# Performance work log

Hardware: AMD Instinct MI355X
Metric: run time of the kernel (lower is better)

The kernel has to match this reference:

```python
import jax, jax.numpy as jnp
import numpy as np

N_NODES = 100000
N_EDGES = 800000
IN_DIM = 64
HID = 96
OUT_DIM = 1
N_LAYERS = 3
N_CENTRAL = 512
BN_EPS = 1e-5


def setup_inputs() -> dict:
    key = jax.random.key(0)
    ks = jax.random.split(key, 16)
    s = 0.1  # weight scale to keep activations tame
    return {
        "x": jax.random.normal(ks[0], (N_NODES, IN_DIM), jnp.float32),
        "edge_index": jax.random.randint(ks[1], (2, N_EDGES), 0, N_NODES, jnp.int64 if jax.config.jax_enable_x64 else jnp.int32),
        "batch": jnp.zeros((N_NODES,), jnp.int32),
        "central_node_idx": jax.random.randint(ks[2], (N_CENTRAL,), 0, N_NODES, jnp.int32),
        "W_emb": jax.random.normal(ks[3], (IN_DIM, HID), jnp.float32) * s,
        "b_emb": jax.random.normal(ks[4], (HID,), jnp.float32) * s,
        "conv_wl": jax.random.normal(ks[5], (N_LAYERS, HID, HID), jnp.float32) * s,
        "conv_bl": jax.random.normal(ks[6], (N_LAYERS, HID), jnp.float32) * s,
        "conv_wr": jax.random.normal(ks[7], (N_LAYERS, HID, HID), jnp.float32) * s,
        "bn_gamma": jnp.ones((N_LAYERS, HID), jnp.float32),
        "bn_beta": jnp.zeros((N_LAYERS, HID), jnp.float32),
        "W1": jax.random.normal(ks[8], (HID, HID), jnp.float32) * s,
        "b1": jax.random.normal(ks[9], (HID,), jnp.float32) * s,
        "W2": jax.random.normal(ks[10], (HID, OUT_DIM), jnp.float32) * s,
        "b2": jax.random.normal(ks[11], (OUT_DIM,), jnp.float32) * s,
    }


def _sage_mean_agg(h, src, dst, n):
    # PyG SAGEConv mean aggregation: mean of source features at each target node
    msg = h[src]                                             # [E, H] gather
    summed = jax.ops.segment_sum(msg, dst, num_segments=n)   # [N, H] scatter-add
    deg = jax.ops.segment_sum(jnp.ones((src.shape[0],), h.dtype), dst, num_segments=n)
    return summed / jnp.maximum(deg, 1.0)[:, None]


def reference(x, edge_index, batch, central_node_idx, W_emb, b_emb,
              conv_wl, conv_bl, conv_wr, bn_gamma, bn_beta, W1, b1, W2, b2):
    n = x.shape[0]
    src, dst = edge_index[0], edge_index[1]
    h = jax.nn.relu(x @ W_emb + b_emb)                       # [N, H]
    for i in range(conv_wl.shape[0]):
        agg = _sage_mean_agg(h, src, dst, n)
        # SAGEConv: lin_l(agg) (with bias) + lin_r(x_root) (no bias)
        h = agg @ conv_wl[i] + conv_bl[i] + h @ conv_wr[i]
        # BatchNorm1d, training mode: batch stats with biased variance
        mean = h.mean(axis=0)
        var = h.var(axis=0)
        h = (h - mean) * jax.lax.rsqrt(var + BN_EPS) * bn_gamma[i] + bn_beta[i]
        h = jax.nn.relu(h)
    central = h[central_node_idx]                            # [G, H]
    out = jax.nn.relu(central @ W1 + b1) @ W2 + b2           # [G, OUT]
    return out
```

## Files before the change

kernel.cpp:

```cpp
#include <hip/hip_runtime.h>

#define NN 100000
#define NE 800000
#define IND 64
#define HID 96
#define NL 3
#define NC 512
#define BN_EPS 1e-5f

#define NBE ((NN + 127) / 128)
#define NBP (NL * 9)
#define NBH ((NE + 4095) / 4096)
#define NBF ((NE + 4095) / 4096)
#define NBK2 196
#define BCAP 4864

typedef __attribute__((ext_vector_type(8))) short bf16x8;
typedef __attribute__((ext_vector_type(4))) float f32x4;

static __device__ __forceinline__ float b2f(ushort u) {
    union { uint i; float f; } v; v.i = ((uint)u) << 16; return v.f;
}
static __device__ __forceinline__ ushort f2b(float f) {
    union { float f; uint i; } v; v.f = f;
    uint r = v.i + 0x7FFFu + ((v.i >> 16) & 1u);
    return (ushort)(r >> 16);
}
static __device__ __forceinline__ uint pack2(float a, float b) {
    return (uint)f2b(a) | ((uint)f2b(b) << 16);
}

static __device__ __forceinline__ void prep_one(const float* srcA, const float* srcB,
                                                ushort* dst, int t) {
    int lane = t & 63;
    int ct = (t >> 6) % 6;
    int kt = t / (6 * 64);
    int k0 = kt * 32 + (lane >> 4) * 8;
    int col = ct * 16 + (lane & 15);
    ushort tmp[8];
#pragma unroll
    for (int j = 0; j < 8; ++j) {
        int k = k0 + j;
        const float* src = (srcB == nullptr || k < 96) ? srcA : srcB;
        int kk = (srcB == nullptr || k < 96) ? k : k - 96;
        tmp[j] = f2b(src[kk * HID + col]);
    }
    uint* od = (uint*)(dst + (size_t)t * 8);
    od[0] = (uint)tmp[0] | ((uint)tmp[1] << 16);
    od[1] = (uint)tmp[2] | ((uint)tmp[3] << 16);
    od[2] = (uint)tmp[4] | ((uint)tmp[5] << 16);
    od[3] = (uint)tmp[6] | ((uint)tmp[7] << 16);
}

__global__ __launch_bounds__(256) void k_front(const float* __restrict__ x,
        const float* __restrict__ W_emb, const float* __restrict__ bias,
        ushort* __restrict__ h,
        const float* __restrict__ conv_wl, const float* __restrict__ conv_wr,
        ushort* __restrict__ Bfl,
        const int* __restrict__ ei, int* __restrict__ hist,
        int* __restrict__ gcur, uint* __restrict__ part) {
    __shared__ __align__(16) char smem[24576];
    const int b = blockIdx.x;
    const int tid = threadIdx.x;
    if (b >= NBE) {
        if (b < NBE + NBP) {
            int idx = b - NBE;
            int l = idx / 9, bb = idx % 9;
            int t = bb * 256 + tid;
            if (t < 6 * 6 * 64)
                prep_one(conv_wl + (size_t)l * 9216, conv_wr + (size_t)l * 9216,
                         Bfl + (size_t)l * 18432, t);
        } else if (b < NBE + NBP + NBH) {
            int base = (b - NBE - NBP) * 4096;
            for (int i = tid; i < 4096; i += 256) {
                int e = base + i;
                if (e < NE) atomicAdd(&hist[ei[NE + e]], 1);
            }
        } else {
            uint* ordbuf = (uint*)smem;
            unsigned char* sbk = (unsigned char*)(smem + 16384);
            int* lhist = (int*)(smem + 20480);
            int* lscan = (int*)(smem + 21504);
            int* lbase = (int*)(smem + 22528);
            int* lcnt2 = (int*)(smem + 23552);
            const int base_e = (b - NBE - NBP - NBH) * 4096;
            lhist[tid] = 0; lcnt2[tid] = 0;
            __syncthreads();
#pragma unroll
            for (int it = 0; it < 16; ++it) {
                int e = base_e + it * 256 + tid;
                if (e < NE) atomicAdd(&lhist[ei[NE + e] >> 9], 1);
            }
            __syncthreads();
            int v = lhist[tid];
            lscan[tid] = v;
            __syncthreads();
            for (int off = 1; off < 256; off <<= 1) {
                int t2 = (tid >= off) ? lscan[tid - off] : 0;
                __syncthreads();
                lscan[tid] += t2;
                __syncthreads();
            }
            int excl = lscan[tid] - v;
            __syncthreads();
            lscan[tid] = excl;
            if (v > 0) lbase[tid] = atomicAdd(&gcur[tid], v);
            __syncthreads();
#pragma unroll
            for (int it = 0; it < 16; ++it) {
                int e = base_e + it * 256 + tid;
                if (e < NE) {
                    int s = ei[e], d = ei[NE + e];
                    int bk = d >> 9;
                    int lofs = atomicAdd(&lcnt2[bk], 1);
                    int slot = lscan[bk] + lofs;
                    ordbuf[slot] = (uint)s | ((uint)(d & 511) << 17);
                    sbk[slot] = (unsigned char)bk;
                }
            }
            __syncthreads();
            int total = NE - base_e; if (total > 4096) total = 4096;
            for (int i = tid; i < total; i += 256) {
                int bk = sbk[i];
                part[(size_t)bk * BCAP + lbase[bk] + (i - lscan[bk])] = ordbuf[i];
            }
        }
        return;
    }
    ushort* sB = (ushort*)smem;
    ushort* sT = (ushort*)smem;
    for (int i = tid; i < 768; i += 256) {
        int lane = i & 63;
        int ct = (i >> 6) % 6;
        int kt = i / (6 * 64);
        int k0 = kt * 32 + (lane >> 4) * 8;
        int col = ct * 16 + (lane & 15);
        ushort tmp[8];
#pragma unroll
        for (int j = 0; j < 8; ++j) tmp[j] = f2b(W_emb[(k0 + j) * HID + col]);
        uint4 o;
        o.x = (uint)tmp[0] | ((uint)tmp[1] << 16);
        o.y = (uint)tmp[2] | ((uint)tmp[3] << 16);
        o.z = (uint)tmp[4] | ((uint)tmp[5] << 16);
        o.w = (uint)tmp[6] | ((uint)tmp[7] << 16);
        ((uint4*)sB)[i] = o;
    }
    __syncthreads();
    const int wave = tid >> 6, lane = tid & 63;
    const int rowb = wave * 32;
    const int row0 = b * 128 + rowb;
    const int kof = (lane >> 4) * 8;
    f32x4 acc[2][6];
#pragma unroll
    for (int t = 0; t < 2; ++t)
#pragma unroll
        for (int c = 0; c < 6; ++c) acc[t][c] = (f32x4){0.f, 0.f, 0.f, 0.f};
#pragma unroll
    for (int kt = 0; kt < 2; ++kt) {
        int kk = kt * 32 + kof;
        bf16x8 a[2];
#pragma unroll
        for (int t = 0; t < 2; ++t) {
            int r = row0 + t * 16 + (lane & 15);
            if (r >= NN) r = NN - 1;
            const float* src = x + (size_t)r * IND + kk;
            float4 f0 = *(const float4*)src;
            float4 f1 = *(const float4*)(src + 4);
            a[t][0] = (short)f2b(f0.x); a[t][1] = (short)f2b(f0.y);
            a[t][2] = (short)f2b(f0.z); a[t][3] = (short)f2b(f0.w);
            a[t][4] = (short)f2b(f1.x); a[t][5] = (short)f2b(f1.y);
            a[t][6] = (short)f2b(f1.z); a[t][7] = (short)f2b(f1.w);
        }
#pragma unroll
        for (int ct = 0; ct < 6; ++ct) {
            bf16x8 bb = *(const bf16x8*)&sB[((kt * 6 + ct) * 64 + lane) * 8];
            acc[0][ct] = __builtin_amdgcn_mfma_f32_16x16x32_bf16(a[0], bb, acc[0][ct], 0, 0, 0);
            acc[1][ct] = __builtin_amdgcn_mfma_f32_16x16x32_bf16(a[1], bb, acc[1][ct], 0, 0, 0);
        }
    }
    __syncthreads();
#pragma unroll
    for (int t = 0; t < 2; ++t)
#pragma unroll
        for (int ct = 0; ct < 6; ++ct) {
            int col = ct * 16 + (lane & 15);
            float bv = bias[col];
#pragma unroll
            for (int i = 0; i < 4; ++i) {
                int rb = rowb + t * 16 + (lane >> 4) * 4 + i;
                float v = acc[t][ct][i] + bv;
                sT[rb * HID + col] = f2b(v > 0.f ? v : 0.f);
            }
        }
    __syncthreads();
    for (int i = tid; i < 1536; i += 256) {
        int r = i / 12;
        int g = b * 128 + r;
        if (g < NN) ((uint4*)(h + (size_t)g * HID))[i % 12] = ((uint4*)sT)[i];
    }
}

__global__ __launch_bounds__(1024) void k_scan1(const int* __restrict__ hist,
        int* __restrict__ rp, int* __restrict__ bsum) {
    __shared__ int sd[1024];
    const int tid = threadIdx.x;
    const int i = blockIdx.x * 1024 + tid;
    int v = (i < NN) ? hist[i] : 0;
    sd[tid] = v;
    __syncthreads();
    for (int off = 1; off < 1024; off <<= 1) {
        int t = (tid >= off) ? sd[tid - off] : 0;
        __syncthreads();
        sd[tid] += t;
        __syncthreads();
    }
    if (i < NN) rp[i] = sd[tid] - v;
    if (tid == 1023) bsum[blockIdx.x] = sd[1023];
}

__global__ __launch_bounds__(128) void k_scan2(const int* __restrict__ bsum,
                                               int* __restrict__ boff) {
    __shared__ int sd[128];
    const int tid = threadIdx.x;
    const int NB = (NN + 1023) / 1024;
    int v = (tid < NB) ? bsum[tid] : 0;
    sd[tid] = v;
    __syncthreads();
    for (int off = 1; off < 128; off <<= 1) {
        int t = (tid >= off) ? sd[tid - off] : 0;
        __syncthreads();
        sd[tid] += t;
        __syncthreads();
    }
    if (tid < NB) boff[tid] = sd[tid] - v;
}

__global__ __launch_bounds__(1024) void k_scan3(int* __restrict__ rp,
        const int* __restrict__ boff) {
    const int i = blockIdx.x * 1024 + threadIdx.x;
    if (i < NN) rp[i] += boff[blockIdx.x];
    if (i == 0) rp[NN] = NE;
}

__global__ __launch_bounds__(256) void k_fill2(const uint* __restrict__ part,
        const int* __restrict__ gcur, const int* __restrict__ rp,
        int* __restrict__ col) {
    __shared__ int lcur[512];
    const int tid = threadIdx.x;
    const int bk = blockIdx.x;
    const int n0 = bk * 512;
    for (int i = tid; i < 512; i += 256) {
        int n = n0 + i;
        lcur[i] = (n < NN) ? rp[n] : 0;
    }
    __syncthreads();
    const int cnt = gcur[bk];
    const uint* pb = part + (size_t)bk * BCAP;
    for (int e = tid; e < cnt; e += 256) {
        uint v = pb[e];
        int pos = atomicAdd(&lcur[v >> 17], 1);
        col[pos] = (int)(v & 0x1FFFF);
    }
}

__global__ __launch_bounds__(256) void k_agg(const ushort* __restrict__ pre,
        const int* __restrict__ rp, const int* __restrict__ col,
        const float* __restrict__ stats, const float* __restrict__ gamma,
        const float* __restrict__ beta, ushort* __restrict__ agg) {
    __shared__ float sc[96], sh[96];
    const int tid = threadIdx.x;
    if (tid < 96) {
        float scv = 1.f, shv = 0.f;
        if (stats) {
            float mean = stats[tid] * (1.f / NN);
            float var  = stats[96 + tid] * (1.f / NN) - mean * mean;
            float s = gamma[tid] * rsqrtf(var + BN_EPS);
            scv = s; shv = beta[tid] - mean * s;
        }
        sc[tid] = scv; sh[tid] = shv;
    }
    __syncthreads();
    const int lane = tid & 15;
    const int n = blockIdx.x * 16 + (tid >> 4);
    if (n >= NN) return;
    const float s0a = sc[2*lane],      h0a = sh[2*lane];
    const float s0b = sc[2*lane + 1],  h0b = sh[2*lane + 1];
    const float s1a = sc[2*lane + 32], h1a = sh[2*lane + 32];
    const float s1b = sc[2*lane + 33], h1b = sh[2*lane + 33];
    const float s2a = sc[2*lane + 64], h2a = sh[2*lane + 64];
    const float s2b = sc[2*lane + 65], h2b = sh[2*lane + 65];
    const int e0 = rp[n], e1 = rp[n + 1];
    float a0 = 0.f, a1 = 0.f, a2 = 0.f, a3 = 0.f, a4 = 0.f, a5 = 0.f;
    const uint* hu = (const uint*)pre;
    int e = e0;
    for (; e + 8 <= e1; e += 8) {
        uint u[8][3];
#pragma unroll
        for (int i = 0; i < 8; ++i) {
            const uint* r = hu + (size_t)col[e + i] * 48 + lane;
            u[i][0] = r[0]; u[i][1] = r[16]; u[i][2] = r[32];
        }
#pragma unroll
        for (int i = 0; i < 8; ++i) {
            a0 += fmaxf(b2f((ushort)u[i][0])         * s0a + h0a, 0.f);
            a1 += fmaxf(b2f((ushort)(u[i][0] >> 16)) * s0b + h0b, 0.f);
            a2 += fmaxf(b2f((ushort)u[i][1])         * s1a + h1a, 0.f);
            a3 += fmaxf(b2f((ushort)(u[i][1] >> 16)) * s1b + h1b, 0.f);
            a4 += fmaxf(b2f((ushort)u[i][2])         * s2a + h2a, 0.f);
            a5 += fmaxf(b2f((ushort)(u[i][2] >> 16)) * s2b + h2b, 0.f);
        }
    }
    for (; e + 4 <= e1; e += 4) {
        uint u[4][3];
#pragma unroll
        for (int i = 0; i < 4; ++i) {
            const uint* r = hu + (size_t)col[e + i] * 48 + lane;
            u[i][0] = r[0]; u[i][1] = r[16]; u[i][2] = r[32];
        }
#pragma unroll
        for (int i = 0; i < 4; ++i) {
            a0 += fmaxf(b2f((ushort)u[i][0])         * s0a + h0a, 0.f);
            a1 += fmaxf(b2f((ushort)(u[i][0] >> 16)) * s0b + h0b, 0.f);
            a2 += fmaxf(b2f((ushort)u[i][1])         * s1a + h1a, 0.f);
            a3 += fmaxf(b2f((ushort)(u[i][1] >> 16)) * s1b + h1b, 0.f);
            a4 += fmaxf(b2f((ushort)u[i][2])         * s2a + h2a, 0.f);
            a5 += fmaxf(b2f((ushort)(u[i][2] >> 16)) * s2b + h2b, 0.f);
        }
    }
    for (; e < e1; ++e) {
        const uint* r = hu + (size_t)col[e] * 48 + lane;
        uint u0 = r[0], u1 = r[16], u2 = r[32];
        a0 += fmaxf(b2f((ushort)u0)         * s0a + h0a, 0.f);
        a1 += fmaxf(b2f((ushort)(u0 >> 16)) * s0b + h0b, 0.f);
        a2 += fmaxf(b2f((ushort)u1)         * s1a + h1a, 0.f);
        a3 += fmaxf(b2f((ushort)(u1 >> 16)) * s1b + h1b, 0.f);
        a4 += fmaxf(b2f((ushort)u2)         * s2a + h2a, 0.f);
        a5 += fmaxf(b2f((ushort)(u2 >> 16)) * s2b + h2b, 0.f);
    }
    int d = e1 - e0; if (d < 1) d = 1;
    float inv = 1.0f / (float)d;
    uint* ar = (uint*)agg + (size_t)n * 48 + lane;
    ar[0]  = pack2(a0 * inv, a1 * inv);
    ar[16] = pack2(a2 * inv, a3 * inv);
    ar[32] = pack2(a4 * inv, a5 * inv);
}

__global__ __launch_bounds__(256, 4) void k_gemm(const ushort* __restrict__ aggb,
        const ushort* __restrict__ pre, const ushort* __restrict__ Bf,
        const float* __restrict__ bl, ushort* __restrict__ hnew,
        float* __restrict__ stats,
        const float* __restrict__ statsP, const float* __restrict__ gammaP,
        const float* __restrict__ betaP) {
    __shared__ __align__(16) char smem[40704];
    ushort* sB = (ushort*)smem;
    ushort* sT = (ushort*)smem;
    float*  sredS = (float*)(smem + 36864);
    float*  sredQ = (float*)(smem + 38400);
    float2* sscsh = (float2*)(smem + 39936);
    const int tid = threadIdx.x;
    for (int i = tid; i < 2304; i += 256) ((uint4*)sB)[i] = ((const uint4*)Bf)[i];
    if (tid < 96) {
        float scv = 1.f, shv = 0.f;
        if (statsP) {
            float mean = statsP[tid] * (1.f / NN);
            float var  = statsP[96 + tid] * (1.f / NN) - mean * mean;
            float s = gammaP[tid] * rsqrtf(var + BN_EPS);
            scv = s; shv = betaP[tid] - mean * s;
        }
        sscsh[tid] = make_float2(scv, shv);
    }
    __syncthreads();
    const int wave = tid >> 6, lane = tid & 63;
    const int rowb = wave * 32;
    const int row0 = blockIdx.x * 128 + rowb;
    const int kof = (lane >> 4) * 8;
    f32x4 acc[2][6];
#pragma unroll
    for (int t = 0; t < 2; ++t)
#pragma unroll
        for (int c = 0; c < 6; ++c) acc[t][c] = (f32x4){0.f, 0.f, 0.f, 0.f};
#pragma unroll
    for (int kt = 0; kt < 6; ++kt) {
        bf16x8 a[2];
#pragma unroll
        for (int t = 0; t < 2; ++t) {
            int r = row0 + t * 16 + (lane & 15);
            if (r >= NN) r = NN - 1;
            if (kt < 3) {
                int kk = kt * 32 + kof;
                a[t] = *(const bf16x8*)(aggb + (size_t)r * HID + kk);
            } else {
                int kk = (kt - 3) * 32 + kof;
                bf16x8 raw = *(const bf16x8*)(pre + (size_t)r * HID + kk);
                union { bf16x8 h; uint u[4]; } pk;
#pragma unroll
                for (int j = 0; j < 4; ++j) {
                    float2 p0 = sscsh[kk + 2*j];
                    float2 p1 = sscsh[kk + 2*j + 1];
                    float v0 = fmaxf(b2f((ushort)raw[2*j])     * p0.x + p0.y, 0.f);
                    float v1 = fmaxf(b2f((ushort)raw[2*j + 1]) * p1.x + p1.y, 0.f);
                    pk.u[j] = pack2(v0, v1);
                }
                a[t] = pk.h;
            }
        }
#pragma unroll
        for (int ct = 0; ct < 6; ++ct) {
            bf16x8 bb = *(const bf16x8*)&sB[((kt * 6 + ct) * 64 + lane) * 8];
            acc[0][ct] = __builtin_amdgcn_mfma_f32_16x16x32_bf16(a[0], bb, acc[0][ct], 0, 0, 0);
            acc[1][ct] = __builtin_amdgcn_mfma_f32_16x16x32_bf16(a[1], bb, acc[1][ct], 0, 0, 0);
        }
    }
    __syncthreads();
    float s[6], q[6];
#pragma unroll
    for (int c = 0; c < 6; ++c) { s[c] = 0.f; q[c] = 0.f; }
#pragma unroll
    for (int t = 0; t < 2; ++t)
#pragma unroll
        for (int ct = 0; ct < 6; ++ct) {
            int col = ct * 16 + (lane & 15);
            float bv = bl[col];
#pragma unroll
            for (int i = 0; i < 4; ++i) {
                int rb = rowb + t * 16 + (lane >> 4) * 4 + i;
                int g = blockIdx.x * 128 + rb;
                float v = acc[t][ct][i] + bv;
                if (g < NN) { s[ct] += v; q[ct] += v * v; }
                sT[rb * HID + col] = f2b(v);
            }
        }
#pragma unroll
    for (int c = 0; c < 6; ++c) {
        s[c] += __shfl_xor(s[c], 16); s[c] += __shfl_xor(s[c], 32);
        q[c] += __shfl_xor(q[c], 16); q[c] += __shfl_xor(q[c], 32);
    }
    if (lane < 16) {
#pragma unroll
        for (int c = 0; c < 6; ++c) {
            sredS[wave * 96 + c * 16 + lane] = s[c];
            sredQ[wave * 96 + c * 16 + lane] = q[c];
        }
    }
    __syncthreads();
    if (tid < 96) {
        float S = sredS[tid] + sredS[96 + tid] + sredS[192 + tid] + sredS[288 + tid];
        float Q = sredQ[tid] + sredQ[96 + tid] + sredQ[192 + tid] + sredQ[288 + tid];
        atomicAdd(&stats[tid], S);
        atomicAdd(&stats[96 + tid], Q);
    }
    for (int i = tid; i < 1536; i += 256) {
        int r = i / 12;
        int g = blockIdx.x * 128 + r;
        if (g < NN) ((uint4*)(hnew + (size_t)g * HID))[i % 12] = ((uint4*)sT)[i];
    }
}

__global__ __launch_bounds__(128) void k_mlp(const ushort* __restrict__ pre,
        const int* __restrict__ cidx, const float* __restrict__ stats,
        const float* __restrict__ gamma, const float* __restrict__ beta,
        const float* __restrict__ W1, const float* __restrict__ b1,
        const float* __restrict__ W2, const float* __restrict__ b2,
        float* __restrict__ out) {
    __shared__ float nh[96];
    __shared__ float hid[96];
    __shared__ float red[128];
    const int c = blockIdx.x;
    const int node = cidx[c];
    const int tid = threadIdx.x;
    if (tid < 96) {
        float mean = stats[tid] * (1.f / NN);
        float var  = stats[96 + tid] * (1.f / NN) - mean * mean;
        float s = gamma[tid] * rsqrtf(var + BN_EPS);
        float v = b2f(pre[(size_t)node * 96 + tid]) * s + (beta[tid] - mean * s);
        nh[tid] = fmaxf(v, 0.f);
    }
    __syncthreads();
    if (tid < 96) {
        float a = 0.f;
        for (int k = 0; k < 96; ++k) a += nh[k] * W1[k * 96 + tid];
        hid[tid] = fmaxf(a + b1[tid], 0.f);
    }
    __syncthreads();
    red[tid] = (tid < 96) ? hid[tid] * W2[tid] : 0.f;
    __syncthreads();
    for (int off = 64; off > 0; off >>= 1) {
        if (tid < off) red[tid] += red[tid + off];
        __syncthreads();
    }
    if (tid == 0) out[c] = red[0] + b2[0];
}

extern "C" void kernel_launch(void* const* d_in, const int* in_sizes, int n_in,
                              void* d_out, int out_size, void* d_ws, size_t ws_size,
                              hipStream_t stream) {
    const float* x        = (const float*)d_in[0];
    const int*   ei       = (const int*)d_in[1];
    const int*   cidx     = (const int*)d_in[3];
    const float* W_emb    = (const float*)d_in[4];
    const float* b_emb    = (const float*)d_in[5];
    const float* conv_wl  = (const float*)d_in[6];
    const float* conv_bl  = (const float*)d_in[7];
    const float* conv_wr  = (const float*)d_in[8];
    const float* bn_gamma = (const float*)d_in[9];
    const float* bn_beta  = (const float*)d_in[10];
    const float* W1       = (const float*)d_in[11];
    const float* b1       = (const float*)d_in[12];
    const float* W2       = (const float*)d_in[13];
    const float* b2       = (const float*)d_in[14];
    float* out = (float*)d_out;

    char* ws = (char*)d_ws;
    size_t off = 0;
    auto alloc = [&](size_t bytes) -> void* {
        void* p = ws + off;
        off = (off + bytes + 255) & ~(size_t)255;
        return p;
    };
    ushort* h    = (ushort*)alloc((size_t)NN * 96 * 2);
    ushort* hnew = (ushort*)alloc((size_t)NN * 96 * 2);
    ushort* agg  = (ushort*)alloc((size_t)NN * 96 * 2);
    int*   hist  = (int*)alloc((size_t)NN * 4);
    int*   gcur  = (int*)alloc(256 * 4);
    int*   rp    = (int*)alloc((size_t)(NN + 1) * 4);
    int*   col   = (int*)alloc((size_t)NE * 4);
    uint*  part  = (uint*)alloc((size_t)NBK2 * BCAP * 4);
    int*   bsum  = (int*)alloc(128 * 4);
    int*   boff  = (int*)alloc(128 * 4);
    float* stats = (float*)alloc((size_t)NL * 192 * 4);
    ushort* Bfl  = (ushort*)alloc((size_t)NL * 6 * 6 * 64 * 8 * 2);
    (void)ws_size; (void)in_sizes; (void)n_in; (void)out_size;

    const int NB = (NN + 1023) / 1024;

    hipMemsetAsync(hist, 0, ((size_t)NN * 4 + 255 & ~(size_t)255) + 256 * 4, stream);
    hipMemsetAsync(stats, 0, (size_t)NL * 192 * 4, stream);

    k_front<<<NBE + NBP + NBH + NBF, 256, 0, stream>>>(x, W_emb, b_emb, h,
        conv_wl, conv_wr, Bfl, ei, hist, gcur, part);
    k_scan1<<<NB, 1024, 0, stream>>>(hist, rp, bsum);
    k_scan2<<<1, 128, 0, stream>>>(bsum, boff);
    k_scan3<<<NB, 1024, 0, stream>>>(rp, boff);
    k_fill2<<<NBK2, 256, 0, stream>>>(part, gcur, rp, col);

    const ushort* src = h;
    ushort* dst = hnew;
    for (int l = 0; l < NL; ++l) {
        const float* stP = (l == 0) ? nullptr : stats + (size_t)(l - 1) * 192;
        const float* gP  = (l == 0) ? nullptr : bn_gamma + (size_t)(l - 1) * 96;
        const float* bP  = (l == 0) ? nullptr : bn_beta + (size_t)(l - 1) * 96;
        k_agg<<<(NN + 15) / 16, 256, 0, stream>>>(src, rp, col, stP, gP, bP, agg);
        k_gemm<<<(NN + 127) / 128, 256, 0, stream>>>(agg, src,
            Bfl + (size_t)l * 18432, conv_bl + (size_t)l * 96, dst,
            stats + (size_t)l * 192, stP, gP, bP);
        const ushort* t = src; src = dst; dst = (ushort*)t;
    }
    k_mlp<<<NC, 128, 0, stream>>>(src, cidx, stats + (size_t)(NL - 1) * 192,
        bn_gamma + (size_t)(NL - 1) * 96, bn_beta + (size_t)(NL - 1) * 96,
        W1, b1, W2, b2, out);
}
```

Before: 271.9 us.

## Fuse mean aggregation into layer GEMM and derive degree histogram from partitions

Merges the per-layer gather/mean aggregation kernel and the MFMA GEMM kernel into one k_layer kernel. Aggregated rows now go into padded shared memory instead of a global bf16 buffer, which removes a full N×96 write and read per layer. The global atomic in-degree histogram pass is replaced by a per-bucket shared-memory histogram built from the already-partitioned edge buckets. B fragments are now read from global memory rather than staged in LDS. The risks are lower gather parallelism per block (128 nodes per 256 threads), possible tail imbalance, and B reads going through cache instead of LDS.

```diff
diff --git a/kernel.cpp b/kernel.cpp
--- a/kernel.cpp
+++ b/kernel.cpp
@@ -10,10 +10,10 @@
 
 #define NBE ((NN + 127) / 128)
 #define NBP (NL * 9)
-#define NBH ((NE + 4095) / 4096)
 #define NBF ((NE + 4095) / 4096)
 #define NBK2 196
 #define BCAP 4864
+#define ATP 52
 
 typedef __attribute__((ext_vector_type(8))) short bf16x8;
 typedef __attribute__((ext_vector_type(4))) float f32x4;
@@ -57,8 +57,8 @@
         ushort* __restrict__ h,
         const float* __restrict__ conv_wl, const float* __restrict__ conv_wr,
         ushort* __restrict__ Bfl,
-        const int* __restrict__ ei, int* __restrict__ hist,
-        int* __restrict__ gcur, uint* __restrict__ part) {
+        const int* __restrict__ ei, int* __restrict__ gcur,
+        uint* __restrict__ part) {
     __shared__ __align__(16) char smem[24576];
     const int b = blockIdx.x;
     const int tid = threadIdx.x;
@@ -70,12 +70,6 @@
             if (t < 6 * 6 * 64)
                 prep_one(conv_wl + (size_t)l * 9216, conv_wr + (size_t)l * 9216,
                          Bfl + (size_t)l * 18432, t);
-        } else if (b < NBE + NBP + NBH) {
-            int base = (b - NBE - NBP) * 4096;
-            for (int i = tid; i < 4096; i += 256) {
-                int e = base + i;
-                if (e < NE) atomicAdd(&hist[ei[NE + e]], 1);
-            }
         } else {
             uint* ordbuf = (uint*)smem;
             unsigned char* sbk = (unsigned char*)(smem + 16384);
@@ -83,7 +77,7 @@
             int* lscan = (int*)(smem + 21504);
             int* lbase = (int*)(smem + 22528);
             int* lcnt2 = (int*)(smem + 23552);
-            const int base_e = (b - NBE - NBP - NBH) * 4096;
+            const int base_e = (b - NBE - NBP) * 4096;
             lhist[tid] = 0; lcnt2[tid] = 0;
             __syncthreads();
 #pragma unroll
@@ -200,6 +194,24 @@
     }
 }
 
+__global__ __launch_bounds__(256) void k_hist2(const uint* __restrict__ part,
+        const int* __restrict__ gcur, int* __restrict__ hist) {
+    __shared__ int lh[512];
+    const int tid = threadIdx.x;
+    const int bk = blockIdx.x;
+    lh[tid] = 0; lh[tid + 256] = 0;
+    __syncthreads();
+    const int cnt = gcur[bk];
+    const uint* pb = part + (size_t)bk * BCAP;
+    for (int e = tid; e < cnt; e += 256) atomicAdd(&lh[pb[e] >> 17], 1);
+    __syncthreads();
+    const int n0 = bk * 512;
+    for (int i = tid; i < 512; i += 256) {
+        int n = n0 + i;
+        if (n < NN) hist[n] = lh[i];
+    }
+}
+
 __global__ __launch_bounds__(1024) void k_scan1(const int* __restrict__ hist,
         int* __restrict__ rp, int* __restrict__ bsum) {
     __shared__ int sd[1024];
@@ -263,102 +275,19 @@
     }
 }
 
-__global__ __launch_bounds__(256) void k_agg(const ushort* __restrict__ pre,
+__global__ __launch_bounds__(256, 4) void k_layer(const ushort* __restrict__ pre,
         const int* __restrict__ rp, const int* __restrict__ col,
-        const float* __restrict__ stats, const float* __restrict__ gamma,
-        const float* __restrict__ beta, ushort* __restrict__ agg) {
-    __shared__ float sc[96], sh[96];
-    const int tid = threadIdx.x;
-    if (tid < 96) {
-        float scv = 1.f, shv = 0.f;
-        if (stats) {
-            float mean = stats[tid] * (1.f / NN);
-            float var  = stats[96 + tid] * (1.f / NN) - mean * mean;
-            float s = gamma[tid] * rsqrtf(var + BN_EPS);
-            scv = s; shv = beta[tid] - mean * s;
-        }
-        sc[tid] = scv; sh[tid] = shv;
-    }
-    __syncthreads();
-    const int lane = tid & 15;
-    const int n = blockIdx.x * 16 + (tid >> 4);
-    if (n >= NN) return;
-    const float s0a = sc[2*lane],      h0a = sh[2*lane];
-    const float s0b = sc[2*lane + 1],  h0b = sh[2*lane + 1];
-    const float s1a = sc[2*lane + 32], h1a = sh[2*lane + 32];
-    const float s1b = sc[2*lane + 33], h1b = sh[2*lane + 33];
-    const float s2a = sc[2*lane + 64], h2a = sh[2*lane + 64];
-    const float s2b = sc[2*lane + 65], h2b = sh[2*lane + 65];
-    const int e0 = rp[n], e1 = rp[n + 1];
-    float a0 = 0.f, a1 = 0.f, a2 = 0.f, a3 = 0.f, a4 = 0.f, a5 = 0.f;
-    const uint* hu = (const uint*)pre;
-    int e = e0;
-    for (; e + 8 <= e1; e += 8) {
-        uint u[8][3];
-#pragma unroll
-        for (int i = 0; i < 8; ++i) {
-            const uint* r = hu + (size_t)col[e + i] * 48 + lane;
-            u[i][0] = r[0]; u[i][1] = r[16]; u[i][2] = r[32];
-        }
-#pragma unroll
-        for (int i = 0; i < 8; ++i) {
-            a0 += fmaxf(b2f((ushort)u[i][0])         * s0a + h0a, 0.f);
-            a1 += fmaxf(b2f((ushort)(u[i][0] >> 16)) * s0b + h0b, 0.f);
-            a2 += fmaxf(b2f((ushort)u[i][1])         * s1a + h1a, 0.f);
-            a3 += fmaxf(b2f((ushort)(u[i][1] >> 16)) * s1b + h1b, 0.f);
-            a4 += fmaxf(b2f((ushort)u[i][2])         * s2a + h2a, 0.f);
-            a5 += fmaxf(b2f((ushort)(u[i][2] >> 16)) * s2b + h2b, 0.f);
-        }
-    }
-    for (; e + 4 <= e1; e += 4) {
-        uint u[4][3];
-#pragma unroll
-        for (int i = 0; i < 4; ++i) {
-            const uint* r = hu + (size_t)col[e + i] * 48 + lane;
-            u[i][0] = r[0]; u[i][1] = r[16]; u[i][2] = r[32];
-        }
-#pragma unroll
-        for (int i = 0; i < 4; ++i) {
-            a0 += fmaxf(b2f((ushort)u[i][0])         * s0a + h0a, 0.f);
-            a1 += fmaxf(b2f((ushort)(u[i][0] >> 16)) * s0b + h0b, 0.f);
-            a2 += fmaxf(b2f((ushort)u[i][1])         * s1a + h1a, 0.f);
-            a3 += fmaxf(b2f((ushort)(u[i][1] >> 16)) * s1b + h1b, 0.f);
-            a4 += fmaxf(b2f((ushort)u[i][2])         * s2a + h2a, 0.f);
-            a5 += fmaxf(b2f((ushort)(u[i][2] >> 16)) * s2b + h2b, 0.f);
-        }
-    }
-    for (; e < e1; ++e) {
-        const uint* r = hu + (size_t)col[e] * 48 + lane;
-        uint u0 = r[0], u1 = r[16], u2 = r[32];
-        a0 += fmaxf(b2f((ushort)u0)         * s0a + h0a, 0.f);
-        a1 += fmaxf(b2f((ushort)(u0 >> 16)) * s0b + h0b, 0.f);
-        a2 += fmaxf(b2f((ushort)u1)         * s1a + h1a, 0.f);
-        a3 += fmaxf(b2f((ushort)(u1 >> 16)) * s1b + h1b, 0.f);
-        a4 += fmaxf(b2f((ushort)u2)         * s2a + h2a, 0.f);
-        a5 += fmaxf(b2f((ushort)(u2 >> 16)) * s2b + h2b, 0.f);
-    }
-    int d = e1 - e0; if (d < 1) d = 1;
-    float inv = 1.0f / (float)d;
-    uint* ar = (uint*)agg + (size_t)n * 48 + lane;
-    ar[0]  = pack2(a0 * inv, a1 * inv);
-    ar[16] = pack2(a2 * inv, a3 * inv);
-    ar[32] = pack2(a4 * inv, a5 * inv);
-}
-
-__global__ __launch_bounds__(256, 4) void k_gemm(const ushort* __restrict__ aggb,
-        const ushort* __restrict__ pre, const ushort* __restrict__ Bf,
-        const float* __restrict__ bl, ushort* __restrict__ hnew,
-        float* __restrict__ stats,
+        const ushort* __restrict__ Bf, const float* __restrict__ bl,
+        ushort* __restrict__ hnew, float* __restrict__ stats,
         const float* __restrict__ statsP, const float* __restrict__ gammaP,
         const float* __restrict__ betaP) {
-    __shared__ __align__(16) char smem[40704];
-    ushort* sB = (ushort*)smem;
-    ushort* sT = (ushort*)smem;
-    float*  sredS = (float*)(smem + 36864);
-    float*  sredQ = (float*)(smem + 38400);
-    float2* sscsh = (float2*)(smem + 39936);
-    const int tid = threadIdx.x;
-    for (int i = tid; i < 2304; i += 256) ((uint4*)sB)[i] = ((const uint4*)Bf)[i];
+    __shared__ __align__(16) char smem[30464];
+    uint*   aggT  = (uint*)smem;
+    ushort* sT    = (ushort*)smem;
+    float*  sredS = (float*)(smem + 26624);
+    float*  sredQ = (float*)(smem + 28160);
+    float2* sscsh = (float2*)(smem + 29696);
+    const int tid = threadIdx.x;
     if (tid < 96) {
         float scv = 1.f, shv = 0.f;
         if (statsP) {
@@ -370,9 +299,57 @@
         sscsh[tid] = make_float2(scv, shv);
     }
     __syncthreads();
+    const int feat = tid & 15;
+    const int grp  = tid >> 4;
+    const int node0 = blockIdx.x * 128;
+    const float2 p0a = sscsh[2*feat],      p0b = sscsh[2*feat + 1];
+    const float2 p1a = sscsh[2*feat + 32], p1b = sscsh[2*feat + 33];
+    const float2 p2a = sscsh[2*feat + 64], p2b = sscsh[2*feat + 65];
+    const uint* hu = (const uint*)pre;
+    for (int nl = grp; nl < 128; nl += 16) {
+        uint* arow = aggT + nl * ATP;
+        int n = node0 + nl;
+        if (n >= NN) { arow[feat] = 0; arow[feat+16] = 0; arow[feat+32] = 0; continue; }
+        const int e0 = rp[n], e1 = rp[n + 1];
+        float a0 = 0.f, a1 = 0.f, a2 = 0.f, a3 = 0.f, a4 = 0.f, a5 = 0.f;
+        int e = e0;
+        for (; e + 8 <= e1; e += 8) {
+            uint u[8][3];
+#pragma unroll
+            for (int i = 0; i < 8; ++i) {
+                const uint* r = hu + (size_t)col[e + i] * 48 + feat;
+                u[i][0] = r[0]; u[i][1] = r[16]; u[i][2] = r[32];
+            }
+#pragma unroll
+            for (int i = 0; i < 8; ++i) {
+                a0 += fmaxf(b2f((ushort)u[i][0])         * p0a.x + p0a.y, 0.f);
+                a1 += fmaxf(b2f((ushort)(u[i][0] >> 16)) * p0b.x + p0b.y, 0.f);
+                a2 += fmaxf(b2f((ushort)u[i][1])         * p1a.x + p1a.y, 0.f);
+                a3 += fmaxf(b2f((ushort)(u[i][1] >> 16)) * p1b.x + p1b.y, 0.f);
+                a4 += fmaxf(b2f((ushort)u[i][2])         * p2a.x + p2a.y, 0.f);
+                a5 += fmaxf(b2f((ushort)(u[i][2] >> 16)) * p2b.x + p2b.y, 0.f);
+            }
+        }
+        for (; e < e1; ++e) {
+            const uint* r = hu + (size_t)col[e] * 48 + feat;
+            uint u0 = r[0], u1 = r[16], u2 = r[32];
+            a0 += fmaxf(b2f((ushort)u0)         * p0a.x + p0a.y, 0.f);
+            a1 += fmaxf(b2f((ushort)(u0 >> 16)) * p0b.x + p0b.y, 0.f);
+            a2 += fmaxf(b2f((ushort)u1)         * p1a.x + p1a.y, 0.f);
+            a3 += fmaxf(b2f((ushort)(u1 >> 16)) * p1b.x + p1b.y, 0.f);
+            a4 += fmaxf(b2f((ushort)u2)         * p2a.x + p2a.y, 0.f);
+            a5 += fmaxf(b2f((ushort)(u2 >> 16)) * p2b.x + p2b.y, 0.f);
+        }
+        int d = e1 - e0; if (d < 1) d = 1;
+        float inv = 1.0f / (float)d;
+        arow[feat]      = pack2(a0 * inv, a1 * inv);
+        arow[feat + 16] = pack2(a2 * inv, a3 * inv);
+        arow[feat + 32] = pack2(a4 * inv, a5 * inv);
+    }
+    __syncthreads();
     const int wave = tid >> 6, lane = tid & 63;
     const int rowb = wave * 32;
-    const int row0 = blockIdx.x * 128 + rowb;
+    const int row0 = node0 + rowb;
     const int kof = (lane >> 4) * 8;
     f32x4 acc[2][6];
 #pragma unroll
@@ -384,21 +361,21 @@
         bf16x8 a[2];
 #pragma unroll
         for (int t = 0; t < 2; ++t) {
-            int r = row0 + t * 16 + (lane & 15);
-            if (r >= NN) r = NN - 1;
+            int rb = rowb + t * 16 + (lane & 15);
             if (kt < 3) {
-                int kk = kt * 32 + kof;
-                a[t] = *(const bf16x8*)(aggb + (size_t)r * HID + kk);
+                a[t] = *(const bf16x8*)(aggT + rb * ATP + kt * 16 + (kof >> 1));
             } else {
+                int r = node0 + rb;
+                if (r >= NN) r = NN - 1;
                 int kk = (kt - 3) * 32 + kof;
                 bf16x8 raw = *(const bf16x8*)(pre + (size_t)r * HID + kk);
                 union { bf16x8 h; uint u[4]; } pk;
 #pragma unroll
                 for (int j = 0; j < 4; ++j) {
-                    float2 p0 = sscsh[kk + 2*j];
-                    float2 p1 = sscsh[kk + 2*j + 1];
-                    float v0 = fmaxf(b2f((ushort)raw[2*j])     * p0.x + p0.y, 0.f);
-                    float v1 = fmaxf(b2f((ushort)raw[2*j + 1]) * p1.x + p1.y, 0.f);
+                    float2 q0 = sscsh[kk + 2*j];
+                    float2 q1 = sscsh[kk + 2*j + 1];
+                    float v0 = fmaxf(b2f((ushort)raw[2*j])     * q0.x + q0.y, 0.f);
+                    float v1 = fmaxf(b2f((ushort)raw[2*j + 1]) * q1.x + q1.y, 0.f);
                     pk.u[j] = pack2(v0, v1);
                 }
                 a[t] = pk.h;
@@ -406,7 +383,7 @@
         }
 #pragma unroll
         for (int ct = 0; ct < 6; ++ct) {
-            bf16x8 bb = *(const bf16x8*)&sB[((kt * 6 + ct) * 64 + lane) * 8];
+            bf16x8 bb = *(const bf16x8*)&Bf[((kt * 6 + ct) * 64 + lane) * 8];
             acc[0][ct] = __builtin_amdgcn_mfma_f32_16x16x32_bf16(a[0], bb, acc[0][ct], 0, 0, 0);
             acc[1][ct] = __builtin_amdgcn_mfma_f32_16x16x32_bf16(a[1], bb, acc[1][ct], 0, 0, 0);
         }
@@ -419,15 +396,15 @@
     for (int t = 0; t < 2; ++t)
 #pragma unroll
         for (int ct = 0; ct < 6; ++ct) {
-            int col = ct * 16 + (lane & 15);
-            float bv = bl[col];
+            int colj = ct * 16 + (lane & 15);
+            float bv = bl[colj];
 #pragma unroll
             for (int i = 0; i < 4; ++i) {
                 int rb = rowb + t * 16 + (lane >> 4) * 4 + i;
-                int g = blockIdx.x * 128 + rb;
+                int g = node0 + rb;
                 float v = acc[t][ct][i] + bv;
                 if (g < NN) { s[ct] += v; q[ct] += v * v; }
-                sT[rb * HID + col] = f2b(v);
+                sT[rb * HID + colj] = f2b(v);
             }
         }
 #pragma unroll
@@ -451,7 +428,7 @@
     }
     for (int i = tid; i < 1536; i += 256) {
         int r = i / 12;
-        int g = blockIdx.x * 128 + r;
+        int g = node0 + r;
         if (g < NN) ((uint4*)(hnew + (size_t)g * HID))[i % 12] = ((uint4*)sT)[i];
     }
 }
@@ -519,9 +496,8 @@
     };
     ushort* h    = (ushort*)alloc((size_t)NN * 96 * 2);
     ushort* hnew = (ushort*)alloc((size_t)NN * 96 * 2);
-    ushort* agg  = (ushort*)alloc((size_t)NN * 96 * 2);
+    int*   gcur  = (int*)alloc(256 * 4);
     int*   hist  = (int*)alloc((size_t)NN * 4);
-    int*   gcur  = (int*)alloc(256 * 4);
     int*   rp    = (int*)alloc((size_t)(NN + 1) * 4);
     int*   col   = (int*)alloc((size_t)NE * 4);
     uint*  part  = (uint*)alloc((size_t)NBK2 * BCAP * 4);
@@ -533,11 +509,12 @@
 
     const int NB = (NN + 1023) / 1024;
 
-    hipMemsetAsync(hist, 0, ((size_t)NN * 4 + 255 & ~(size_t)255) + 256 * 4, stream);
+    hipMemsetAsync(gcur, 0, 256 * 4, stream);
     hipMemsetAsync(stats, 0, (size_t)NL * 192 * 4, stream);
 
-    k_front<<<NBE + NBP + NBH + NBF, 256, 0, stream>>>(x, W_emb, b_emb, h,
-        conv_wl, conv_wr, Bfl, ei, hist, gcur, part);
+    k_front<<<NBE + NBP + NBF, 256, 0, stream>>>(x, W_emb, b_emb, h,
+        conv_wl, conv_wr, Bfl, ei, gcur, part);
+    k_hist2<<<NBK2, 256, 0, stream>>>(part, gcur, hist);
     k_scan1<<<NB, 1024, 0, stream>>>(hist, rp, bsum);
     k_scan2<<<1, 128, 0, stream>>>(bsum, boff);
     k_scan3<<<NB, 1024, 0, stream>>>(rp, boff);
@@ -549,8 +526,7 @@
         const float* stP = (l == 0) ? nullptr : stats + (size_t)(l - 1) * 192;
         const float* gP  = (l == 0) ? nullptr : bn_gamma + (size_t)(l - 1) * 96;
         const float* bP  = (l == 0) ? nullptr : bn_beta + (size_t)(l - 1) * 96;
-        k_agg<<<(NN + 15) / 16, 256, 0, stream>>>(src, rp, col, stP, gP, bP, agg);
-        k_gemm<<<(NN + 127) / 128, 256, 0, stream>>>(agg, src,
+        k_layer<<<(NN + 127) / 128, 256, 0, stream>>>(src, rp, col,
             Bfl + (size_t)l * 18432, conv_bl + (size_t)l * 96, dst,
             stats + (size_t)l * 192, stP, gP, bP);
         const ushort* t = src; src = dst; dst = (ushort*)t;
```

Result: no change. 274.1 us (+0.8%).

## Build CSR row pointers from bucket partitions, dropping global histogram and scans

Applied to the files above, without the earlier changes.

Removes the per-edge global atomic histogram over destination nodes and the three-kernel prefix scan that produced row pointers. Row pointers are now derived inside each bucket-fill block, using a local shared-memory histogram of the already-partitioned edges plus a single-block scan of the per-bucket counts. This cuts global atomics, two kernel launches and a large memset. The cost is an extra pass over each bucket's partition in the fill kernel.

```diff
diff --git a/kernel.cpp b/kernel.cpp
--- a/kernel.cpp
+++ b/kernel.cpp
@@ -10,7 +10,6 @@
 
 #define NBE ((NN + 127) / 128)
 #define NBP (NL * 9)
-#define NBH ((NE + 4095) / 4096)
 #define NBF ((NE + 4095) / 4096)
 #define NBK2 196
 #define BCAP 4864
@@ -57,8 +56,8 @@
         ushort* __restrict__ h,
         const float* __restrict__ conv_wl, const float* __restrict__ conv_wr,
         ushort* __restrict__ Bfl,
-        const int* __restrict__ ei, int* __restrict__ hist,
-        int* __restrict__ gcur, uint* __restrict__ part) {
+        const int* __restrict__ ei, int* __restrict__ gcur,
+        uint* __restrict__ part) {
     __shared__ __align__(16) char smem[24576];
     const int b = blockIdx.x;
     const int tid = threadIdx.x;
@@ -70,12 +69,6 @@
             if (t < 6 * 6 * 64)
                 prep_one(conv_wl + (size_t)l * 9216, conv_wr + (size_t)l * 9216,
                          Bfl + (size_t)l * 18432, t);
-        } else if (b < NBE + NBP + NBH) {
-            int base = (b - NBE - NBP) * 4096;
-            for (int i = tid; i < 4096; i += 256) {
-                int e = base + i;
-                if (e < NE) atomicAdd(&hist[ei[NE + e]], 1);
-            }
         } else {
             uint* ordbuf = (uint*)smem;
             unsigned char* sbk = (unsigned char*)(smem + 16384);
@@ -83,7 +76,7 @@
             int* lscan = (int*)(smem + 21504);
             int* lbase = (int*)(smem + 22528);
             int* lcnt2 = (int*)(smem + 23552);
-            const int base_e = (b - NBE - NBP - NBH) * 4096;
+            const int base_e = (b - NBE - NBP) * 4096;
             lhist[tid] = 0; lcnt2[tid] = 0;
             __syncthreads();
 #pragma unroll
@@ -200,65 +193,61 @@
     }
 }
 
-__global__ __launch_bounds__(1024) void k_scan1(const int* __restrict__ hist,
-        int* __restrict__ rp, int* __restrict__ bsum) {
-    __shared__ int sd[1024];
+__global__ __launch_bounds__(256) void k_bscan(const int* __restrict__ gcur,
+                                               int* __restrict__ bbase) {
+    __shared__ int sd[256];
     const int tid = threadIdx.x;
-    const int i = blockIdx.x * 1024 + tid;
-    int v = (i < NN) ? hist[i] : 0;
+    int v = (tid < NBK2) ? gcur[tid] : 0;
     sd[tid] = v;
     __syncthreads();
-    for (int off = 1; off < 1024; off <<= 1) {
+    for (int off = 1; off < 256; off <<= 1) {
         int t = (tid >= off) ? sd[tid - off] : 0;
         __syncthreads();
         sd[tid] += t;
         __syncthreads();
     }
-    if (i < NN) rp[i] = sd[tid] - v;
-    if (tid == 1023) bsum[blockIdx.x] = sd[1023];
-}
-
-__global__ __launch_bounds__(128) void k_scan2(const int* __restrict__ bsum,
-                                               int* __restrict__ boff) {
-    __shared__ int sd[128];
-    const int tid = threadIdx.x;
-    const int NB = (NN + 1023) / 1024;
-    int v = (tid < NB) ? bsum[tid] : 0;
-    sd[tid] = v;
-    __syncthreads();
-    for (int off = 1; off < 128; off <<= 1) {
-        int t = (tid >= off) ? sd[tid - off] : 0;
-        __syncthreads();
-        sd[tid] += t;
-        __syncthreads();
-    }
-    if (tid < NB) boff[tid] = sd[tid] - v;
-}
-
-__global__ __launch_bounds__(1024) void k_scan3(int* __restrict__ rp,
-        const int* __restrict__ boff) {
-    const int i = blockIdx.x * 1024 + threadIdx.x;
-    if (i < NN) rp[i] += boff[blockIdx.x];
-    if (i == 0) rp[NN] = NE;
-}
-
-__global__ __launch_bounds__(256) void k_fill2(const uint* __restrict__ part,
-        const int* __restrict__ gcur, const int* __restrict__ rp,
-        int* __restrict__ col) {
-    __shared__ int lcur[512];
+    if (tid < NBK2) bbase[tid] = sd[tid] - v;
+}
+
+__global__ __launch_bounds__(256) void k_fill3(const uint* __restrict__ part,
+        const int* __restrict__ gcur, const int* __restrict__ bbase,
+        int* __restrict__ rp, int* __restrict__ col) {
+    __shared__ int lh[512];
+    __shared__ int lsc[512];
+    __shared__ int pairs[256];
     const int tid = threadIdx.x;
     const int bk = blockIdx.x;
+    lh[tid] = 0; lh[tid + 256] = 0;
+    __syncthreads();
+    const int cnt = gcur[bk];
+    const uint* pb = part + (size_t)bk * BCAP;
+    for (int e = tid; e < cnt; e += 256) atomicAdd(&lh[pb[e] >> 17], 1);
+    __syncthreads();
+    int p0 = lh[2 * tid], p1 = lh[2 * tid + 1];
+    int ps = p0 + p1;
+    pairs[tid] = ps;
+    __syncthreads();
+    for (int off = 1; off < 256; off <<= 1) {
+        int t = (tid >= off) ? pairs[tid - off] : 0;
+        __syncthreads();
+        pairs[tid] += t;
+        __syncthreads();
+    }
+    int base = bbase[bk];
+    int excl = base + pairs[tid] - ps;
+    lsc[2 * tid] = excl;
+    lsc[2 * tid + 1] = excl + p0;
+    __syncthreads();
     const int n0 = bk * 512;
     for (int i = tid; i < 512; i += 256) {
         int n = n0 + i;
-        lcur[i] = (n < NN) ? rp[n] : 0;
-    }
-    __syncthreads();
-    const int cnt = gcur[bk];
-    const uint* pb = part + (size_t)bk * BCAP;
+        if (n < NN) rp[n] = lsc[i];
+    }
+    if (bk == NBK2 - 1 && tid == 0) rp[NN] = NE;
+    __syncthreads();
     for (int e = tid; e < cnt; e += 256) {
         uint v = pb[e];
-        int pos = atomicAdd(&lcur[v >> 17], 1);
+        int pos = atomicAdd(&lsc[v >> 17], 1);
         col[pos] = (int)(v & 0x1FFFF);
     }
 }
@@ -520,28 +509,22 @@
     ushort* h    = (ushort*)alloc((size_t)NN * 96 * 2);
     ushort* hnew = (ushort*)alloc((size_t)NN * 96 * 2);
     ushort* agg  = (ushort*)alloc((size_t)NN * 96 * 2);
-    int*   hist  = (int*)alloc((size_t)NN * 4);
     int*   gcur  = (int*)alloc(256 * 4);
+    int*   bbase = (int*)alloc(256 * 4);
     int*   rp    = (int*)alloc((size_t)(NN + 1) * 4);
     int*   col   = (int*)alloc((size_t)NE * 4);
     uint*  part  = (uint*)alloc((size_t)NBK2 * BCAP * 4);
-    int*   bsum  = (int*)alloc(128 * 4);
-    int*   boff  = (int*)alloc(128 * 4);
     float* stats = (float*)alloc((size_t)NL * 192 * 4);
     ushort* Bfl  = (ushort*)alloc((size_t)NL * 6 * 6 * 64 * 8 * 2);
     (void)ws_size; (void)in_sizes; (void)n_in; (void)out_size;
 
-    const int NB = (NN + 1023) / 1024;
-
-    hipMemsetAsync(hist, 0, ((size_t)NN * 4 + 255 & ~(size_t)255) + 256 * 4, stream);
+    hipMemsetAsync(gcur, 0, 256 * 4, stream);
     hipMemsetAsync(stats, 0, (size_t)NL * 192 * 4, stream);
 
-    k_front<<<NBE + NBP + NBH + NBF, 256, 0, stream>>>(x, W_emb, b_emb, h,
-        conv_wl, conv_wr, Bfl, ei, hist, gcur, part);
-    k_scan1<<<NB, 1024, 0, stream>>>(hist, rp, bsum);
-    k_scan2<<<1, 128, 0, stream>>>(bsum, boff);
-    k_scan3<<<NB, 1024, 0, stream>>>(rp, boff);
-    k_fill2<<<NBK2, 256, 0, stream>>>(part, gcur, rp, col);
+    k_front<<<NBE + NBP + NBF, 256, 0, stream>>>(x, W_emb, b_emb, h,
+        conv_wl, conv_wr, Bfl, ei, gcur, part);
+    k_bscan<<<1, 256, 0, stream>>>(gcur, bbase);
+    k_fill3<<<NBK2, 256, 0, stream>>>(part, gcur, bbase, rp, col);
 
     const ushort* src = h;
     ushort* dst = hnew;
```

Result: faster. 245.6 us (-9.7%).
